# Performance work log

Hardware: AMD Instinct MI355X
Metric: run time of the kernel (lower is better)

Reference implementation:

```python
import jax, jax.numpy as jnp
import numpy as np

B, L, D, F = 4096, 200, 64, 100000


def setup_inputs() -> dict:
    key = jax.random.key(0)
    ks = jax.random.split(key, 12)
    film_hist = jax.random.randint(ks[0], (B, L), 0, F)                 # padded rated-film indices
    ratings = jax.random.uniform(ks[1], (B, L), jnp.float32) * 4.5 + 0.5  # letterboxd-style 0.5..5
    lengths = jax.random.randint(ks[2], (B,), 1, L + 1)                 # ragged history lengths (>=1)
    film_indices = jax.random.randint(ks[3], (B,), 0, F)                # target films to score
    emb_table = jax.random.normal(ks[4], (F, D), jnp.float32) * 0.1
    W1 = jax.random.normal(ks[5], (5 * D, 2 * D), jnp.float32) * 0.05
    b1 = jnp.zeros((2 * D,), jnp.float32)
    W2 = jax.random.normal(ks[6], (2 * D, D), jnp.float32) * 0.05
    b2 = jnp.zeros((D,), jnp.float32)
    W3 = jax.random.normal(ks[7], (D, 1), jnp.float32) * 0.05
    b3 = jnp.zeros((1,), jnp.float32)
    return {"film_hist": film_hist, "ratings": ratings, "lengths": lengths,
            "film_indices": film_indices, "emb_table": emb_table,
            "W1": W1, "b1": b1, "W2": W2, "b2": b2, "W3": W3, "b3": b3}


def _user_embeddings(film_hist, ratings, lengths, emb_table):
    # mask[b, l] = l < lengths[b]
    mask = jnp.arange(L)[None, :] < lengths[:, None]          # [B, L]
    n = lengths.astype(jnp.float32)                           # [B]
    mean_r = jnp.sum(jnp.where(mask, ratings, 0.0), axis=1) / n
    weights = ratings - mean_r[:, None] + 0.1                 # [B, L]
    hist_emb = emb_table[film_hist]                           # [B, L, D]
    w = hist_emb * weights[:, :, None]                        # weighted film embeddings
    m3 = mask[:, :, None]
    wmin = jnp.min(jnp.where(m3, w, jnp.inf), axis=1)
    wmax = jnp.max(jnp.where(m3, w, -jnp.inf), axis=1)
    wmean = jnp.sum(jnp.where(m3, w, 0.0), axis=1) / n[:, None]
    # median: sort valid entries (pads go to +inf at the end); torch.median
    # returns the lower middle element -> index (n-1)//2
    ws = jnp.sort(jnp.where(m3, w, jnp.inf), axis=1)
    mid = ((lengths - 1) // 2)[:, None, None]                 # [B,1,1]
    wmed = jnp.take_along_axis(ws, jnp.broadcast_to(mid, (B, 1, D)), axis=1)[:, 0, :]
    ue = jnp.concatenate([wmin, wmax, wmean, wmed], axis=1)   # [B, 4D]
    return ue / jnp.linalg.norm(ue, axis=1, keepdims=True)


def reference(film_hist, ratings, lengths, film_indices, emb_table, W1, b1, W2, b2, W3, b3):
    ue = _user_embeddings(film_hist, ratings, lengths, emb_table)  # [B, 4D]
    fe = emb_table[film_indices]                                   # [B, D]
    x = jnp.concatenate([ue, fe], axis=1)                          # [B, 5D]
    h = jax.nn.relu(x @ W1 + b1)   # Dropout(0.2) is identity in eval
    h = jax.nn.relu(h @ W2 + b2)
    return jax.nn.sigmoid(h @ W3 + b3)[:, 0]                       # [B]
```

## Files before the change

### kernel.cpp

```cpp
#include <hip/hip_runtime.h>
#include <hip/hip_bf16.h>
#include <stdint.h>


#define B_ 4096
#define L_ 200
#define D_ 64
#define LPAD 224

__device__ __forceinline__ void xpose_sign(uint32_t (&W)[16]) {
  #define XS(k, jj, m) { uint32_t tt = ((W[k] ^ (W[(k)|(jj)] >> (jj))) & (m)); \
                         W[k] ^= tt; W[(k)|(jj)] ^= (tt << (jj)); }
  XS(0,8,0x00FF00FFu) XS(1,8,0x00FF00FFu) XS(2,8,0x00FF00FFu) XS(3,8,0x00FF00FFu)
  XS(4,8,0x00FF00FFu) XS(5,8,0x00FF00FFu) XS(6,8,0x00FF00FFu) XS(7,8,0x00FF00FFu)
  XS(0,4,0x0F0F0F0Fu) XS(1,4,0x0F0F0F0Fu) XS(2,4,0x0F0F0F0Fu) XS(3,4,0x0F0F0F0Fu)
  XS(8,4,0x0F0F0F0Fu) XS(9,4,0x0F0F0F0Fu) XS(10,4,0x0F0F0F0Fu) XS(11,4,0x0F0F0F0Fu)
  XS(0,2,0x33333333u) XS(1,2,0x33333333u) XS(4,2,0x33333333u) XS(5,2,0x33333333u)
  XS(8,2,0x33333333u) XS(9,2,0x33333333u) XS(12,2,0x33333333u) XS(13,2,0x33333333u)
  XS(0,1,0x55555555u) XS(2,1,0x55555555u) XS(4,1,0x55555555u) XS(6,1,0x55555555u)
  XS(8,1,0x55555555u) XS(10,1,0x55555555u) XS(12,1,0x55555555u) XS(14,1,0x55555555u)
  #undef XS
  const uint32_t S = W[0];
  W[0] = ~S;
  #pragma unroll
  for (int j = 1; j < 16; ++j) W[j] ^= S;
}

template<bool TWO>
__device__ __forceinline__ uint32_t select_med(
    const uint32_t (&W0)[16], const uint32_t (&W1x)[16],
    uint32_t a0, uint32_t a1, int k)
{
  uint32_t prefix = 0;
  #pragma unroll
  for (int bb = 15; bb >= 0; --bb) {
    const uint32_t z0 = a0 & ~W0[15 - bb];
    int cnt = __popc(z0);
    uint32_t z1 = 0u;
    if (TWO) {
      z1 = a1 & ~W1x[15 - bb];
      cnt += __popc(z1);
    }
    cnt += __builtin_amdgcn_update_dpp(0, cnt, 0xB1, 0xF, 0xF, true);
    cnt += __builtin_amdgcn_update_dpp(0, cnt, 0x4E, 0xF, 0xF, true);
    const bool zs = (k < cnt);
    a0 = zs ? z0 : (a0 ^ z0);
    if (TWO) a1 = zs ? z1 : (a1 ^ z1);
    k      = zs ? k : (k - cnt);
    prefix = zs ? prefix : (prefix | (1u << bb));
  }
  return prefix;
}

__global__ __launch_bounds__(256) void stats_kernel(
    const int* __restrict__ film_hist,
    const float* __restrict__ ratings,
    const int* __restrict__ lengths,
    const int* __restrict__ film_indices,
    const float* __restrict__ emb,
    float* __restrict__ x)
{
  __shared__ uint2 pair_s[LPAD];
  __shared__ float red[4];
  __shared__ float ue[4*D_];

  const int t = threadIdx.x;
  const int wv = t >> 6;
  const int lane = t & 63;
  const int d = t >> 2;
  const int sub = t & 3;
  const int b = blockIdx.x;
  const int n = lengths[b];

  const int fi = film_indices[b];
  const float fev = (t < 64) ? emb[(size_t)fi * D_ + t] : 0.f;

  float r = 0.f;
  if (t < LPAD) {
    uint2 e;
    if (t < n) {
      e.x = ((uint32_t)film_hist[(size_t)b*L_ + t]) << 8;
      r = ratings[(size_t)b*L_ + t];
      e.y = __float_as_uint(r);
    } else {
      e.x = 0u; e.y = 0u;
    }
    pair_s[t] = e;
  }
  float s = r;
  #pragma unroll
  for (int off = 32; off; off >>= 1) s += __shfl_down(s, off);
  if (lane == 0) red[wv] = s;
  __syncthreads();
  const float mr1 = 0.1f - (red[0]+red[1]+red[2]+red[3]) / (float)n;

  if (t < n) pair_s[t].y = __float_as_uint(r + mr1);
  __syncthreads();

  const char* eb = (const char*)emb;
  const uint32_t d4 = (uint32_t)d * 4u;
  float vmin = __builtin_inff(), vmax = -__builtin_inff(), vsum = 0.f;
  uint32_t W0[16], W1x[16];
  #pragma unroll
  for (int j = 0; j < 16; ++j) { W0[j] = 0u; W1x[j] = 0u; }

  const int ng    = (n + 15) >> 4;
  const int nfull = n >> 4;

  #define LDSP(G, PE) { \
    _Pragma("unroll") \
    for (int j = 0; j < 4; ++j) PE[j] = pair_s[sub + 16*(G) + 4*j]; }
  #define VMEMG(PE, EV) { \
    _Pragma("unroll") \
    for (int j = 0; j < 4; ++j) \
      EV[j] = *(const float*)(eb + (PE[j].x + d4)); }
  #define CONSG(G, EV, PE) { \
    uint32_t kk[4]; \
    _Pragma("unroll") \
    for (int j = 0; j < 4; ++j) { \
      const float w_ = EV[j] * __uint_as_float(PE[j].y); \
      vsum += w_;                       \
      kk[j] = __float_as_uint(w_); \
    } \
    if ((G) < nfull) { \
      _Pragma("unroll") \
      for (int j = 0; j < 4; ++j) { \
        const float w_ = __uint_as_float(kk[j]); \
        vmin = fminf(vmin, w_); vmax = fmaxf(vmax, w_); \
      } \
    } else { \
      _Pragma("unroll") \
      for (int j = 0; j < 4; ++j) { \
        const int l_ = sub + 16*(G) + 4*j; \
        const float w_ = __uint_as_float(kk[j]); \
        vmin = fminf(vmin, (l_ < n) ? w_ :  __builtin_inff()); \
        vmax = fmaxf(vmax, (l_ < n) ? w_ : -__builtin_inff()); \
      } \
    } \
    const uint32_t wA_ = __builtin_amdgcn_perm(kk[1], kk[0], 0x07060302u); \
    const uint32_t wB_ = __builtin_amdgcn_perm(kk[3], kk[2], 0x07060302u); \
    if ((G) < 8) { W0[2*(G)]      = wA_; W0[2*(G)+1]      = wB_; } \
    else         { W1x[2*((G)-8)] = wA_; W1x[2*((G)-8)+1] = wB_; } }

  uint2 peA[4], peB[4];
  float evA[4], evB[4];
  LDSP(0, peA); VMEMG(peA, evA);
  #pragma unroll
  for (int gp = 0; gp < 7; ++gp) {
    const int g = 2*gp;
    if (g < ng) {
      if (g+1 < ng) { LDSP(g+1, peB); VMEMG(peB, evB); }
      CONSG(g, evA, peA);
      if (g+2 < ng) { LDSP(g+2, peA); VMEMG(peA, evA); }
      if (g+1 < ng) { CONSG(g+1, evB, peB); }
    }
  }
  #undef LDSP
  #undef VMEMG
  #undef CONSG

  vmin = fminf(vmin, __shfl_xor(vmin, 1));
  vmin = fminf(vmin, __shfl_xor(vmin, 2));
  vmax = fmaxf(vmax, __shfl_xor(vmax, 1));
  vmax = fmaxf(vmax, __shfl_xor(vmax, 2));
  vsum += __shfl_xor(vsum, 1);
  vsum += __shfl_xor(vsum, 2);

  const bool two = (n > 128);
  xpose_sign(W0);
  if (two) xpose_sign(W1x);

  const int cth = (n > sub) ? ((n - sub + 3) >> 2) : 0;
  const int v0 = (cth < 32) ? cth : 32;
  const int v1 = cth - v0;
  const int ce0 = (v0 + 1) >> 1, cf0 = v0 >> 1;
  uint32_t a0 = ((1u << ce0) - 1u) << (16 - ce0);
  if (cf0) a0 |= ((1u << cf0) - 1u) << (32 - cf0);
  const int ce1 = (v1 + 1) >> 1, cf1 = v1 >> 1;
  uint32_t a1 = ((1u << ce1) - 1u) << (16 - ce1);
  if (cf1) a1 |= ((1u << cf1) - 1u) << (32 - cf1);
  if (v1 == 0) a1 = 0u;

  const int k = (n - 1) >> 1;
  const uint32_t prefix = two ? select_med<true >(W0, W1x, a0, a1, k)
                              : select_med<false>(W0, W1x, a0, a1, k);

  if (sub == 0) {
    uint32_t key32 = (prefix << 16) | 0x8000u;
    const float med = (prefix & 0x8000u) ? __uint_as_float(key32 ^ 0x80000000u)
                                         : __uint_as_float(~key32);
    ue[d]       = vmin;
    ue[64 + d]  = vmax;
    ue[128 + d] = vsum / (float)n;
    ue[192 + d] = med;
  }
  __syncthreads();

  const float vv = ue[t];
  float ss = vv * vv;
  #pragma unroll
  for (int off = 32; off; off >>= 1) ss += __shfl_down(ss, off);
  if (lane == 0) red[wv] = ss;
  __syncthreads();
  const float rn = 1.0f / sqrtf(red[0]+red[1]+red[2]+red[3]);

  float* xb = x + (size_t)b * 320;
  xb[t] = vv * rn;
  if (t < 64) xb[256 + t] = fev;
}

#define U_ 8

__global__ __launch_bounds__(256) void mlp_kernel(
    const float* __restrict__ x,
    const float* __restrict__ W1, const float* __restrict__ b1,
    const float* __restrict__ W2, const float* __restrict__ b2,
    const float* __restrict__ W3, const float* __restrict__ b3,
    float* __restrict__ out)
{
  __shared__ float xs[U_*320];
  __shared__ float h1s[U_*128];
  __shared__ float h2s[U_*64];
  const int t = threadIdx.x;
  const int u0 = blockIdx.x * U_;

  for (int i = t; i < U_*80; i += 256)
    ((float4*)xs)[i] = ((const float4*)(x + (size_t)u0*320))[i];
  __syncthreads();

  {
    const int j = t & 127, g = t >> 7;
    const int ub = g*4;
    float acc[4];
    const float bj = b1[j];
    #pragma unroll
    for (int q = 0; q < 4; ++q) acc[q] = bj;
    for (int i = 0; i < 320; i += 4) {
      float w0 = W1[(i+0)*128 + j];
      float w1 = W1[(i+1)*128 + j];
      float w2 = W1[(i+2)*128 + j];
      float w3 = W1[(i+3)*128 + j];
      #pragma unroll
      for (int q = 0; q < 4; ++q) {
        float4 xv = *(const float4*)&xs[(ub+q)*320 + i];
        acc[q] += xv.x*w0 + xv.y*w1 + xv.z*w2 + xv.w*w3;
      }
    }
    #pragma unroll
    for (int q = 0; q < 4; ++q) h1s[(ub+q)*128 + j] = fmaxf(acc[q], 0.f);
  }
  __syncthreads();

  {
    const int j = t & 63, g = t >> 6;
    const int ub = g*2;
    float acc[2];
    const float bj = b2[j];
    acc[0] = bj; acc[1] = bj;
    for (int i = 0; i < 128; i += 4) {
      float w0 = W2[(i+0)*64 + j];
      float w1 = W2[(i+1)*64 + j];
      float w2 = W2[(i+2)*64 + j];
      float w3 = W2[(i+3)*64 + j];
      #pragma unroll
      for (int q = 0; q < 2; ++q) {
        float4 hv = *(const float4*)&h1s[(ub+q)*128 + i];
        acc[q] += hv.x*w0 + hv.y*w1 + hv.z*w2 + hv.w*w3;
      }
    }
    #pragma unroll
    for (int q = 0; q < 2; ++q) h2s[(ub+q)*64 + j] = fmaxf(acc[q], 0.f);
  }
  __syncthreads();

  if (t < U_*4) {
    const int u = t >> 2, sub = t & 3;
    float a = 0.f;
    #pragma unroll
    for (int i = 0; i < 16; ++i) a += h2s[u*64 + sub*16 + i] * W3[sub*16 + i];
    a += __shfl_xor(a, 1);
    a += __shfl_xor(a, 2);
    if (sub == 0) out[u0 + u] = 1.f / (1.f + __expf(-(a + b3[0])));
  }
}

extern "C" void kernel_launch(void* const* d_in, const int* in_sizes, int n_in,
                              void* d_out, int out_size, void* d_ws, size_t ws_size,
                              hipStream_t stream) {
  const int*   film_hist = (const int*)d_in[0];
  const float* ratings   = (const float*)d_in[1];
  const int*   lengths   = (const int*)d_in[2];
  const int*   film_idx  = (const int*)d_in[3];
  const float* emb       = (const float*)d_in[4];
  const float* W1 = (const float*)d_in[5];
  const float* b1 = (const float*)d_in[6];
  const float* W2 = (const float*)d_in[7];
  const float* b2 = (const float*)d_in[8];
  const float* W3 = (const float*)d_in[9];
  const float* b3 = (const float*)d_in[10];

  float* xbuf = (float*)d_ws;
  float* outp = (float*)d_out;

  stats_kernel<<<B_, 256, 0, stream>>>(film_hist, ratings, lengths, film_idx, emb, xbuf);
  mlp_kernel<<<B_/U_, 256, 0, stream>>>(xbuf, W1, b1, W2, b2, W3, b3, outp);
}
```

Before: 52.82 us.

## Fuse user-stats and MLP kernels into one per-user kernel

Merges the statistics kernel and the MLP kernel into a single launch, so each block computes its user's normalized features in shared memory and then runs the three MLP layers for that one user. This removes the second launch and the round trip of the 320-float feature buffer through global memory. In exchange, every block re-reads W1 (about 160 KB) and W2 from cache for a single user instead of amortizing them over 8 users. The matvec is split across thread halves and quarters with partial sums combined in shared memory.

Result: slower. 54.24 us (+2.7%).

```diff
diff --git a/kernel.cpp b/kernel.cpp
--- a/kernel.cpp
+++ b/kernel.cpp
@@ -52,17 +52,22 @@
   return prefix;
 }
 
-__global__ __launch_bounds__(256) void stats_kernel(
+__global__ __launch_bounds__(256) void fused_kernel(
     const int* __restrict__ film_hist,
     const float* __restrict__ ratings,
     const int* __restrict__ lengths,
     const int* __restrict__ film_indices,
     const float* __restrict__ emb,
-    float* __restrict__ x)
+    const float* __restrict__ W1, const float* __restrict__ b1,
+    const float* __restrict__ W2, const float* __restrict__ b2,
+    const float* __restrict__ W3, const float* __restrict__ b3,
+    float* __restrict__ out)
 {
   __shared__ uint2 pair_s[LPAD];
   __shared__ float red[4];
-  __shared__ float ue[4*D_];
+  __shared__ float xls[320];
+  __shared__ float ph[256];
+  __shared__ float h1s[128];
 
   const int t = threadIdx.x;
   const int wv = t >> 6;
@@ -71,9 +76,6 @@
   const int sub = t & 3;
   const int b = blockIdx.x;
   const int n = lengths[b];
-
-  const int fi = film_indices[b];
-  const float fev = (t < 64) ? emb[(size_t)fi * D_ + t] : 0.f;
 
   float r = 0.f;
   if (t < LPAD) {
@@ -87,6 +89,10 @@
     }
     pair_s[t] = e;
   }
+  if (t >= 192) {
+    const int fi = film_indices[b];
+    xls[256 + (t - 192)] = emb[(size_t)fi * D_ + (t - 192)];
+  }
   float s = r;
   #pragma unroll
   for (int off = 32; off; off >>= 1) s += __shfl_down(s, off);
@@ -100,9 +106,9 @@
   const char* eb = (const char*)emb;
   const uint32_t d4 = (uint32_t)d * 4u;
   float vmin = __builtin_inff(), vmax = -__builtin_inff(), vsum = 0.f;
-  uint32_t W0[16], W1x[16];
-  #pragma unroll
-  for (int j = 0; j < 16; ++j) { W0[j] = 0u; W1x[j] = 0u; }
+  uint32_t W0[16], W1p[16];
+  #pragma unroll
+  for (int j = 0; j < 16; ++j) { W0[j] = 0u; W1p[j] = 0u; }
 
   const int ng    = (n + 15) >> 4;
   const int nfull = n >> 4;
@@ -139,8 +145,8 @@
     } \
     const uint32_t wA_ = __builtin_amdgcn_perm(kk[1], kk[0], 0x07060302u); \
     const uint32_t wB_ = __builtin_amdgcn_perm(kk[3], kk[2], 0x07060302u); \
-    if ((G) < 8) { W0[2*(G)]      = wA_; W0[2*(G)+1]      = wB_; } \
-    else         { W1x[2*((G)-8)] = wA_; W1x[2*((G)-8)+1] = wB_; } }
+    if ((G) < 8) { W0[2*(G)]       = wA_; W0[2*(G)+1]       = wB_; } \
+    else         { W1p[2*((G)-8)]  = wA_; W1p[2*((G)-8)+1]  = wB_; } }
 
   uint2 peA[4], peB[4];
   float evA[4], evB[4];
@@ -168,7 +174,7 @@
 
   const bool two = (n > 128);
   xpose_sign(W0);
-  if (two) xpose_sign(W1x);
+  if (two) xpose_sign(W1p);
 
   const int cth = (n > sub) ? ((n - sub + 3) >> 2) : 0;
   const int v0 = (cth < 32) ? cth : 32;
@@ -182,105 +188,63 @@
   if (v1 == 0) a1 = 0u;
 
   const int k = (n - 1) >> 1;
-  const uint32_t prefix = two ? select_med<true >(W0, W1x, a0, a1, k)
-                              : select_med<false>(W0, W1x, a0, a1, k);
+  const uint32_t prefix = two ? select_med<true >(W0, W1p, a0, a1, k)
+                              : select_med<false>(W0, W1p, a0, a1, k);
 
   if (sub == 0) {
     uint32_t key32 = (prefix << 16) | 0x8000u;
     const float med = (prefix & 0x8000u) ? __uint_as_float(key32 ^ 0x80000000u)
                                          : __uint_as_float(~key32);
-    ue[d]       = vmin;
-    ue[64 + d]  = vmax;
-    ue[128 + d] = vsum / (float)n;
-    ue[192 + d] = med;
-  }
-  __syncthreads();
-
-  const float vv = ue[t];
+    xls[d]       = vmin;
+    xls[64 + d]  = vmax;
+    xls[128 + d] = vsum / (float)n;
+    xls[192 + d] = med;
+  }
+  __syncthreads();
+
+  const float vv = xls[t];
   float ss = vv * vv;
   #pragma unroll
   for (int off = 32; off; off >>= 1) ss += __shfl_down(ss, off);
   if (lane == 0) red[wv] = ss;
   __syncthreads();
   const float rn = 1.0f / sqrtf(red[0]+red[1]+red[2]+red[3]);
-
-  float* xb = x + (size_t)b * 320;
-  xb[t] = vv * rn;
-  if (t < 64) xb[256 + t] = fev;
-}
-
-#define U_ 8
-
-__global__ __launch_bounds__(256) void mlp_kernel(
-    const float* __restrict__ x,
-    const float* __restrict__ W1, const float* __restrict__ b1,
-    const float* __restrict__ W2, const float* __restrict__ b2,
-    const float* __restrict__ W3, const float* __restrict__ b3,
-    float* __restrict__ out)
-{
-  __shared__ float xs[U_*320];
-  __shared__ float h1s[U_*128];
-  __shared__ float h2s[U_*64];
-  const int t = threadIdx.x;
-  const int u0 = blockIdx.x * U_;
-
-  for (int i = t; i < U_*80; i += 256)
-    ((float4*)xs)[i] = ((const float4*)(x + (size_t)u0*320))[i];
+  xls[t] = vv * rn;
   __syncthreads();
 
   {
-    const int j = t & 127, g = t >> 7;
-    const int ub = g*4;
-    float acc[4];
-    const float bj = b1[j];
-    #pragma unroll
-    for (int q = 0; q < 4; ++q) acc[q] = bj;
-    for (int i = 0; i < 320; i += 4) {
-      float w0 = W1[(i+0)*128 + j];
-      float w1 = W1[(i+1)*128 + j];
-      float w2 = W1[(i+2)*128 + j];
-      float w3 = W1[(i+3)*128 + j];
-      #pragma unroll
-      for (int q = 0; q < 4; ++q) {
-        float4 xv = *(const float4*)&xs[(ub+q)*320 + i];
-        acc[q] += xv.x*w0 + xv.y*w1 + xv.z*w2 + xv.w*w3;
-      }
-    }
-    #pragma unroll
-    for (int q = 0; q < 4; ++q) h1s[(ub+q)*128 + j] = fmaxf(acc[q], 0.f);
-  }
+    const int j = t & 127, half = t >> 7;
+    const float* Wp = W1 + (size_t)(half*160)*128 + j;
+    const float* xp = xls + half*160;
+    float a0h = 0.f, a1h = 0.f;
+    #pragma unroll 8
+    for (int i = 0; i < 160; i += 2) {
+      a0h += xp[i]   * Wp[(size_t)i*128];
+      a1h += xp[i+1] * Wp[(size_t)(i+1)*128];
+    }
+    ph[half*128 + j] = a0h + a1h;
+  }
+  __syncthreads();
+  if (t < 128) h1s[t] = fmaxf(b1[t] + ph[t] + ph[128 + t], 0.f);
   __syncthreads();
 
   {
     const int j = t & 63, g = t >> 6;
-    const int ub = g*2;
-    float acc[2];
-    const float bj = b2[j];
-    acc[0] = bj; acc[1] = bj;
-    for (int i = 0; i < 128; i += 4) {
-      float w0 = W2[(i+0)*64 + j];
-      float w1 = W2[(i+1)*64 + j];
-      float w2 = W2[(i+2)*64 + j];
-      float w3 = W2[(i+3)*64 + j];
-      #pragma unroll
-      for (int q = 0; q < 2; ++q) {
-        float4 hv = *(const float4*)&h1s[(ub+q)*128 + i];
-        acc[q] += hv.x*w0 + hv.y*w1 + hv.z*w2 + hv.w*w3;
-      }
-    }
+    const float* Wp = W2 + (size_t)(g*32)*64 + j;
+    const float* hp = h1s + g*32;
+    float a = 0.f;
+    #pragma unroll 8
+    for (int i = 0; i < 32; ++i) a += hp[i] * Wp[(size_t)i*64];
+    ph[g*64 + j] = a;
+  }
+  __syncthreads();
+
+  if (t < 64) {
+    const float h = fmaxf(b2[t] + ph[t] + ph[64+t] + ph[128+t] + ph[192+t], 0.f);
+    float acc = h * W3[t];
     #pragma unroll
-    for (int q = 0; q < 2; ++q) h2s[(ub+q)*64 + j] = fmaxf(acc[q], 0.f);
-  }
-  __syncthreads();
-
-  if (t < U_*4) {
-    const int u = t >> 2, sub = t & 3;
-    float a = 0.f;
-    #pragma unroll
-    for (int i = 0; i < 16; ++i) a += h2s[u*64 + sub*16 + i] * W3[sub*16 + i];
-    a += __shfl_xor(a, 1);
-    a += __shfl_xor(a, 2);
-    if (sub == 0) out[u0 + u] = 1.f / (1.f + __expf(-(a + b3[0])));
+    for (int off = 32; off; off >>= 1) acc += __shfl_down(acc, off);
+    if (t == 0) out[b] = 1.f / (1.f + __expf(-(acc + b3[0])));
   }
 }
 
@@ -299,9 +263,6 @@
   const float* W3 = (const float*)d_in[9];
   const float* b3 = (const float*)d_in[10];
 
-  float* xbuf = (float*)d_ws;
-  float* outp = (float*)d_out;
-
-  stats_kernel<<<B_, 256, 0, stream>>>(film_hist, ratings, lengths, film_idx, emb, xbuf);
-  mlp_kernel<<<B_/U_, 256, 0, stream>>>(xbuf, W1, b1, W2, b2, W3, b3, outp);
-}
+  fused_kernel<<<B_, 256, 0, stream>>>(film_hist, ratings, lengths, film_idx, emb,
+                                       W1, b1, W2, b2, W3, b3, (float*)d_out);
+}
```

## Split MLP reduction dimension across threads so each weight load serves all rows

Applied to the files above, without the earlier changes.

In the MLP kernel, each thread now owns one output column and half (layer 1) or a quarter (layer 2) of the reduction range, and accumulates for all 8 rows of the block. Partial sums are combined through a new shared buffer before bias and ReLU are applied. This cuts global weight loads per FMA, since each W element is loaded once per block instead of once per row group, at the cost of extra shared memory, an extra barrier per layer and scalar LDS reads. The final dot product is also spread over 32 lanes with a wave shuffle reduction.

New measurement: 51.49 us (median of 2 runs). 2.5% less time.

```diff
diff --git a/kernel.cpp b/kernel.cpp
--- a/kernel.cpp
+++ b/kernel.cpp
@@ -139,8 +139,8 @@
     } \
     const uint32_t wA_ = __builtin_amdgcn_perm(kk[1], kk[0], 0x07060302u); \
     const uint32_t wB_ = __builtin_amdgcn_perm(kk[3], kk[2], 0x07060302u); \
-    if ((G) < 8) { W0[2*(G)]      = wA_; W0[2*(G)+1]      = wB_; } \
-    else         { W1x[2*((G)-8)] = wA_; W1x[2*((G)-8)+1] = wB_; } }
+    if ((G) < 8) { W0[2*(G)]       = wA_; W0[2*(G)+1]       = wB_; } \
+    else         { W1x[2*((G)-8)]  = wA_; W1x[2*((G)-8)+1]  = wB_; } }
 
   uint2 peA[4], peB[4];
   float evA[4], evB[4];
@@ -219,6 +219,7 @@
     float* __restrict__ out)
 {
   __shared__ float xs[U_*320];
+  __shared__ float ph[2048];
   __shared__ float h1s[U_*128];
   __shared__ float h2s[U_*64];
   const int t = threadIdx.x;
@@ -229,58 +230,55 @@
   __syncthreads();
 
   {
-    const int j = t & 127, g = t >> 7;
-    const int ub = g*4;
-    float acc[4];
-    const float bj = b1[j];
-    #pragma unroll
-    for (int q = 0; q < 4; ++q) acc[q] = bj;
-    for (int i = 0; i < 320; i += 4) {
-      float w0 = W1[(i+0)*128 + j];
-      float w1 = W1[(i+1)*128 + j];
-      float w2 = W1[(i+2)*128 + j];
-      float w3 = W1[(i+3)*128 + j];
+    const int j = t & 127, ih = t >> 7;
+    const float* Wp = W1 + (size_t)(ih*160)*128 + j;
+    const int xo = ih*160;
+    float acc[8];
+    #pragma unroll
+    for (int u = 0; u < U_; ++u) acc[u] = 0.f;
+    #pragma unroll 4
+    for (int i = 0; i < 160; ++i) {
+      const float w = Wp[(size_t)i*128];
       #pragma unroll
-      for (int q = 0; q < 4; ++q) {
-        float4 xv = *(const float4*)&xs[(ub+q)*320 + i];
-        acc[q] += xv.x*w0 + xv.y*w1 + xv.z*w2 + xv.w*w3;
-      }
-    }
-    #pragma unroll
-    for (int q = 0; q < 4; ++q) h1s[(ub+q)*128 + j] = fmaxf(acc[q], 0.f);
+      for (int u = 0; u < U_; ++u) acc[u] += xs[u*320 + xo + i] * w;
+    }
+    #pragma unroll
+    for (int u = 0; u < U_; ++u) ph[ih*1024 + u*128 + j] = acc[u];
+  }
+  __syncthreads();
+  for (int e = t; e < 1024; e += 256) {
+    h1s[e] = fmaxf(b1[e & 127] + ph[e] + ph[1024 + e], 0.f);
   }
   __syncthreads();
 
   {
-    const int j = t & 63, g = t >> 6;
-    const int ub = g*2;
-    float acc[2];
-    const float bj = b2[j];
-    acc[0] = bj; acc[1] = bj;
-    for (int i = 0; i < 128; i += 4) {
-      float w0 = W2[(i+0)*64 + j];
-      float w1 = W2[(i+1)*64 + j];
-      float w2 = W2[(i+2)*64 + j];
-      float w3 = W2[(i+3)*64 + j];
+    const int j2 = t & 63, ih2 = t >> 6;
+    const float* Wp = W2 + (size_t)(ih2*32)*64 + j2;
+    const int ho = ih2*32;
+    float acc[8];
+    #pragma unroll
+    for (int u = 0; u < U_; ++u) acc[u] = 0.f;
+    #pragma unroll 4
+    for (int i = 0; i < 32; ++i) {
+      const float w = Wp[(size_t)i*64];
       #pragma unroll
-      for (int q = 0; q < 2; ++q) {
-        float4 hv = *(const float4*)&h1s[(ub+q)*128 + i];
-        acc[q] += hv.x*w0 + hv.y*w1 + hv.z*w2 + hv.w*w3;
-      }
-    }
-    #pragma unroll
-    for (int q = 0; q < 2; ++q) h2s[(ub+q)*64 + j] = fmaxf(acc[q], 0.f);
-  }
-  __syncthreads();
-
-  if (t < U_*4) {
-    const int u = t >> 2, sub = t & 3;
-    float a = 0.f;
-    #pragma unroll
-    for (int i = 0; i < 16; ++i) a += h2s[u*64 + sub*16 + i] * W3[sub*16 + i];
-    a += __shfl_xor(a, 1);
-    a += __shfl_xor(a, 2);
-    if (sub == 0) out[u0 + u] = 1.f / (1.f + __expf(-(a + b3[0])));
+      for (int u = 0; u < U_; ++u) acc[u] += h1s[u*128 + ho + i] * w;
+    }
+    #pragma unroll
+    for (int u = 0; u < U_; ++u) ph[ih2*512 + u*64 + j2] = acc[u];
+  }
+  __syncthreads();
+  for (int e = t; e < 512; e += 256) {
+    h2s[e] = fmaxf(b2[e & 63] + ph[e] + ph[512 + e] + ph[1024 + e] + ph[1536 + e], 0.f);
+  }
+  __syncthreads();
+
+  {
+    const int u = t >> 5, i = t & 31;
+    float a = h2s[u*64 + i] * W3[i] + h2s[u*64 + 32 + i] * W3[32 + i];
+    #pragma unroll
+    for (int off = 16; off; off >>= 1) a += __shfl_xor(a, off);
+    if (i == 0) out[u0 + u] = 1.f / (1.f + __expf(-(a + b3[0])));
   }
 }
 
```
